# Performance work log

Hardware: AMD Instinct MI355X
Metric: run time of the kernel (lower is better)

The kernel has to match this reference:

```python
import jax, jax.numpy as jnp
from jax import lax
import numpy as np

B, T, H = 4096, 512, 32


def _rnn_layer(xs, h0, Wih, Whh, bih, bhh):
    # xs: [T, B, in], h0: [B, H]. torch RNN tanh: h_t = tanh(x W_ih^T + b_ih + h W_hh^T + b_hh)
    def step(h, x_t):
        h = jnp.tanh(x_t @ Wih.T + bih + h @ Whh.T + bhh)
        return h, h
    h_last, ys = lax.scan(step, h0, xs)
    return ys, h_last  # ys: [T, B, H]


def setup_inputs() -> dict:
    key = jax.random.key(0)
    ks = jax.random.split(key, 12)
    s = 0.1  # keep tanh out of saturation
    return {
        "x": jax.random.normal(ks[0], (B, T, 1), jnp.float32),
        "h_state": jnp.zeros((2, B, H), jnp.float32),
        "Wih0": jax.random.normal(ks[1], (H, 1), jnp.float32) * s,
        "Whh0": jax.random.normal(ks[2], (H, H), jnp.float32) * s,
        "bih0": jax.random.normal(ks[3], (H,), jnp.float32) * s,
        "bhh0": jax.random.normal(ks[4], (H,), jnp.float32) * s,
        "Wih1": jax.random.normal(ks[5], (H, H), jnp.float32) * s,
        "Whh1": jax.random.normal(ks[6], (H, H), jnp.float32) * s,
        "bih1": jax.random.normal(ks[7], (H,), jnp.float32) * s,
        "bhh1": jax.random.normal(ks[8], (H,), jnp.float32) * s,
        "Wfc": jax.random.normal(ks[9], (1, H), jnp.float32) * s,
        "bfc": jax.random.normal(ks[10], (1,), jnp.float32) * s,
    }


def reference(x, h_state, Wih0, Whh0, bih0, bhh0, Wih1, Whh1, bih1, bhh1, Wfc, bfc):
    xs = jnp.transpose(x, (1, 0, 2))  # time-major [T, B, 1]
    ys0, h0_last = _rnn_layer(xs, h_state[0], Wih0, Whh0, bih0, bhh0)
    ys1, h1_last = _rnn_layer(ys0, h_state[1], Wih1, Whh1, bih1, bhh1)
    last = ys1[-1]                      # [B, H] == r_out[:, -1, :]
    pred = (last @ Wfc.T + bfc)[:, 0]   # Linear(32,1) then squeeze(-1) -> [B]
    h_new = jnp.stack([h0_last, h1_last], axis=0)  # [2, B, H]
    return pred, h_new
```

## Files before the change

### kernel.cpp

```cpp
#include <hip/hip_runtime.h>

#define BB 4096
#define TT 512
#define HH 32

typedef _Float16 half8 __attribute__((ext_vector_type(8)));
typedef _Float16 half4 __attribute__((ext_vector_type(4)));
typedef _Float16 h2    __attribute__((ext_vector_type(2)));
typedef float    f32x4 __attribute__((ext_vector_type(4)));

#define MFMA16F(a, b, c) __builtin_amdgcn_mfma_f32_16x16x32_f16((a), (b), (c), 0, 0, 0)

union frag_u { half8 h8; h2 p[4]; };
union h4u   { half4 v;  h2 p[2]; };

__device__ __forceinline__ h2 pkrtz(float a, float b) {
    auto r = __builtin_amdgcn_cvt_pkrtz(a, b);
    union { decltype(r) i; h2 o; } u;
    u.i = r;
    return u.o;
}

__device__ __forceinline__ h2 tanh_h2(h2 v) {
    const h2 LO = {(_Float16)(-2.75f), (_Float16)(-2.75f)};
    const h2 HI = {(_Float16)(2.75f), (_Float16)(2.75f)};
    const h2 C0 = {(_Float16)(0.9976293f), (_Float16)(0.9976293f)};
    const h2 C1 = {(_Float16)(-0.3098016f), (_Float16)(-0.3098016f)};
    const h2 C2 = {(_Float16)(0.0889744f), (_Float16)(0.0889744f)};
    const h2 C3 = {(_Float16)(-0.0163448f), (_Float16)(-0.0163448f)};
    const h2 C4 = {(_Float16)(0.0016113f), (_Float16)(0.0016113f)};
    const h2 C5 = {(_Float16)(-0.00006405f), (_Float16)(-0.00006405f)};
    v = __builtin_elementwise_min(v, HI);
    v = __builtin_elementwise_max(v, LO);
    h2 u = v * v;
    h2 t = __builtin_elementwise_fma(u, C5, C4);
    t = __builtin_elementwise_fma(u, t, C3);
    t = __builtin_elementwise_fma(u, t, C2);
    t = __builtin_elementwise_fma(u, t, C1);
    t = __builtin_elementwise_fma(u, t, C0);
    return v * t;
}

#define XBAR()                                                    \
    do {                                                          \
        asm volatile("s_waitcnt lgkmcnt(0)" ::: "memory");        \
        __builtin_amdgcn_s_barrier();                             \
        asm volatile("" ::: "memory");                            \
    } while (0)

__global__ __launch_bounds__(128) void rnn2_mfma_hs(
    const float* __restrict__ x,
    const float* __restrict__ hstate,
    const float* __restrict__ Wih0,
    const float* __restrict__ Whh0,
    const float* __restrict__ bih0,
    const float* __restrict__ bhh0,
    const float* __restrict__ Wih1,
    const float* __restrict__ Whh1,
    const float* __restrict__ bih1,
    const float* __restrict__ bhh1,
    const float* __restrict__ Wfc,
    const float* __restrict__ bfc,
    float* __restrict__ out)
{
    const int tid = threadIdx.x;
    const int l = tid & 63;
    const int wid = __builtin_amdgcn_readfirstlane(tid >> 6);
    const int q = l >> 4;
    const int n = l & 15;
    const int b = blockIdx.x * 16 + n;
    const bool w0 = (wid == 0);

    __shared__ half4 xbH[2][2][64];

    const int r0 = 8 * (n >> 2) + (n & 3);
    half8 A1i[2], A1h[2];
#pragma unroll
    for (int t = 0; t < 2; ++t) {
        const int row = r0 + 4 * t;
        const float* p1 = Wih1 + row * HH + q * 8;
        const float* p2 = Whh1 + row * HH + q * 8;
        frag_u f1, f2;
#pragma unroll
        for (int jj = 0; jj < 4; ++jj) {
            f1.p[jj] = h2{(_Float16)p1[2 * jj], (_Float16)p1[2 * jj + 1]};
            f2.p[jj] = h2{(_Float16)p2[2 * jj], (_Float16)p2[2 * jj + 1]};
        }
        A1i[t] = f1.h8; A1h[t] = f2.h8;
    }
    half8 A0w;
    {
        const int row = r0 + 4 * wid;
        const float* p0 = Whh0 + row * HH + q * 8;
        frag_u f0;
#pragma unroll
        for (int jj = 0; jj < 4; ++jj)
            f0.p[jj] = h2{(_Float16)p0[2 * jj], (_Float16)p0[2 * jj + 1]};
        A0w = f0.h8;
    }

    float wxs[4], b0s[4], wfc8[8];
#pragma unroll
    for (int r = 0; r < 4; ++r) {
        const int hh = 8 * q + 4 * wid + r;
        wxs[r] = Wih0[hh];
        b0s[r] = bih0[hh] + bhh0[hh];
    }
    f32x4 c1t0, c1t1;
#pragma unroll
    for (int r = 0; r < 4; ++r) {
        c1t0[r] = bih1[8 * q + r] + bhh1[8 * q + r];
        c1t1[r] = bih1[8 * q + 4 + r] + bhh1[8 * q + 4 + r];
    }
#pragma unroll
    for (int j = 0; j < 8; ++j) wfc8[j] = Wfc[8 * q + j];

    frag_u hb0, hb1;
    {
        const float* p0 = hstate + (size_t)b * HH + 8 * q;
        const float* p1 = hstate + (size_t)BB * HH + (size_t)b * HH + 8 * q;
#pragma unroll
        for (int jj = 0; jj < 4; ++jj) {
            hb0.p[jj] = h2{(_Float16)p0[2 * jj], (_Float16)p0[2 * jj + 1]};
            hb1.p[jj] = h2{(_Float16)p1[2 * jj], (_Float16)p1[2 * jj + 1]};
        }
    }

    f32x4 dbp0 = MFMA16F(A1h[0], hb1.h8, c1t0);
    f32x4 dbp1 = MFMA16F(A1h[1], hb1.h8, c1t1);

    const float4* xp = (const float4*)(x + (size_t)b * TT);
    float4 xc = xp[0];

    {
        f32x4 c0;
#pragma unroll
        for (int r = 0; r < 4; ++r) c0[r] = fmaf(wxs[r], xc.x, b0s[r]);
        f32x4 d0 = MFMA16F(A0w, hb0.h8, c0);
        h4u ho;
        ho.p[0] = tanh_h2(pkrtz(d0[0], d0[1]));
        ho.p[1] = tanh_h2(pkrtz(d0[2], d0[3]));
        xbH[wid][0][l] = ho.v;
        XBAR();
        h4u lo, hi;
        lo.v = xbH[0][0][l];
        hi.v = xbH[1][0][l];
        hb0.p[0] = lo.p[0]; hb0.p[1] = lo.p[1];
        hb0.p[2] = hi.p[0]; hb0.p[3] = hi.p[1];
    }

#define STEPB(XT, SLOT)                                                       \
    {                                                                         \
        f32x4 d10 = MFMA16F(A1i[0], hb0.h8, dbp0);                            \
        f32x4 d11 = MFMA16F(A1i[1], hb0.h8, dbp1);                            \
        f32x4 c0;                                                             \
        _Pragma("unroll")                                                     \
        for (int r = 0; r < 4; ++r) c0[r] = fmaf(wxs[r], (XT), b0s[r]);       \
        f32x4 d0 = MFMA16F(A0w, hb0.h8, c0);                                  \
        h4u ho;                                                               \
        ho.p[0] = tanh_h2(pkrtz(d0[0], d0[1]));                               \
        ho.p[1] = tanh_h2(pkrtz(d0[2], d0[3]));                               \
        xbH[wid][SLOT][l] = ho.v;                                             \
        XBAR();                                                               \
        h4u lo, hi;                                                           \
        lo.v = xbH[0][SLOT][l];                                               \
        hi.v = xbH[1][SLOT][l];                                               \
        hb1.p[0] = tanh_h2(pkrtz(d10[0], d10[1]));                            \
        hb1.p[1] = tanh_h2(pkrtz(d10[2], d10[3]));                            \
        hb1.p[2] = tanh_h2(pkrtz(d11[0], d11[1]));                            \
        hb1.p[3] = tanh_h2(pkrtz(d11[2], d11[3]));                            \
        dbp0 = MFMA16F(A1h[0], hb1.h8, c1t0);                                 \
        dbp1 = MFMA16F(A1h[1], hb1.h8, c1t1);                                 \
        hb0.p[0] = lo.p[0]; hb0.p[1] = lo.p[1];                               \
        hb0.p[2] = hi.p[0]; hb0.p[3] = hi.p[1];                               \
    }

    for (int k = 0; k < TT / 4 - 1; ++k) {
        float4 xn = xp[k + 1];
        STEPB(xc.y, 1);
        STEPB(xc.z, 0);
        STEPB(xc.w, 1);
        STEPB(xn.x, 0);
        xc = xn;
    }
    STEPB(xc.y, 1);
    STEPB(xc.z, 0);
    STEPB(xc.w, 1);

    {
        f32x4 d10 = MFMA16F(A1i[0], hb0.h8, dbp0);
        f32x4 d11 = MFMA16F(A1i[1], hb0.h8, dbp1);
        hb1.p[0] = tanh_h2(pkrtz(d10[0], d10[1]));
        hb1.p[1] = tanh_h2(pkrtz(d10[2], d10[3]));
        hb1.p[2] = tanh_h2(pkrtz(d11[0], d11[1]));
        hb1.p[3] = tanh_h2(pkrtz(d11[2], d11[3]));
    }

    float hf0[8], hf1[8];
#pragma unroll
    for (int jj = 0; jj < 4; ++jj) {
        hf0[2 * jj]     = (float)hb0.p[jj].x;
        hf0[2 * jj + 1] = (float)hb0.p[jj].y;
        hf1[2 * jj]     = (float)hb1.p[jj].x;
        hf1[2 * jj + 1] = (float)hb1.p[jj].y;
    }
    if (w0) {
#pragma unroll
        for (int j = 0; j < 8; ++j)
            out[BB + (size_t)b * HH + 8 * q + j] = hf0[j];
    } else {
        float p = 0.f;
#pragma unroll
        for (int j = 0; j < 8; ++j) p = fmaf(wfc8[j], hf1[j], p);
        p += __shfl_xor(p, 16);
        p += __shfl_xor(p, 32);
        if (q == 0) out[b] = p + bfc[0];
#pragma unroll
        for (int j = 0; j < 8; ++j)
            out[BB + (size_t)BB * HH + (size_t)b * HH + 8 * q + j] = hf1[j];
    }
}

extern "C" void kernel_launch(void* const* d_in, const int* in_sizes, int n_in,
                              void* d_out, int out_size, void* d_ws, size_t ws_size,
                              hipStream_t stream) {
    const float* x      = (const float*)d_in[0];
    const float* hstate = (const float*)d_in[1];
    const float* Wih0   = (const float*)d_in[2];
    const float* Whh0   = (const float*)d_in[3];
    const float* bih0   = (const float*)d_in[4];
    const float* bhh0   = (const float*)d_in[5];
    const float* Wih1   = (const float*)d_in[6];
    const float* Whh1   = (const float*)d_in[7];
    const float* bih1   = (const float*)d_in[8];
    const float* bhh1   = (const float*)d_in[9];
    const float* Wfc    = (const float*)d_in[10];
    const float* bfc    = (const float*)d_in[11];
    float* out = (float*)d_out;

    dim3 grid(BB / 16);
    dim3 block(128);
    hipLaunchKernelGGL(rnn2_mfma_hs, grid, block, 0, stream,
                       x, hstate, Wih0, Whh0, bih0, bhh0,
                       Wih1, Whh1, bih1, bhh1, Wfc, bfc, out);
}
```

Before: 204.6 us.

## Split layer-1 recurrence onto a dedicated third wave per block

Blocks grow from two waves to three. Waves 0 and 1 each compute half of the layer-0 hidden state. Wave 2 alone runs the layer-1 MFMAs and tanh on the layer-0 state from the previous step, so the two layers run as a wavefront pipeline. The aim is to take layer-1 work off the critical path of the layer-0 waves at each barrier. In exchange, each block has 50% more waves, wave 2 writes an unused LDS slot every step, and all three waves must still meet at the per-step barrier.

```diff
diff --git a/kernel.cpp b/kernel.cpp
--- a/kernel.cpp
+++ b/kernel.cpp
@@ -48,7 +48,7 @@
         asm volatile("" ::: "memory");                            \
     } while (0)
 
-__global__ __launch_bounds__(128) void rnn2_mfma_hs(
+__global__ __launch_bounds__(192) void rnn2_mfma_pc(
     const float* __restrict__ x,
     const float* __restrict__ hstate,
     const float* __restrict__ Wih0,
@@ -69,11 +69,22 @@
     const int q = l >> 4;
     const int n = l & 15;
     const int b = blockIdx.x * 16 + n;
-    const bool w0 = (wid == 0);
-
-    __shared__ half4 xbH[2][2][64];
+    const bool w2 = (wid == 2);
+
+    __shared__ half4 xbH[3][2][64];
 
     const int r0 = 8 * (n >> 2) + (n & 3);
+    const int ot = wid & 1;
+    half8 A0w;
+    {
+        const int row = r0 + 4 * ot;
+        const float* p0 = Whh0 + row * HH + q * 8;
+        frag_u f0;
+#pragma unroll
+        for (int jj = 0; jj < 4; ++jj)
+            f0.p[jj] = h2{(_Float16)p0[2 * jj], (_Float16)p0[2 * jj + 1]};
+        A0w = f0.h8;
+    }
     half8 A1i[2], A1h[2];
 #pragma unroll
     for (int t = 0; t < 2; ++t) {
@@ -88,21 +99,11 @@
         }
         A1i[t] = f1.h8; A1h[t] = f2.h8;
     }
-    half8 A0w;
-    {
-        const int row = r0 + 4 * wid;
-        const float* p0 = Whh0 + row * HH + q * 8;
-        frag_u f0;
-#pragma unroll
-        for (int jj = 0; jj < 4; ++jj)
-            f0.p[jj] = h2{(_Float16)p0[2 * jj], (_Float16)p0[2 * jj + 1]};
-        A0w = f0.h8;
-    }
 
     float wxs[4], b0s[4], wfc8[8];
 #pragma unroll
     for (int r = 0; r < 4; ++r) {
-        const int hh = 8 * q + 4 * wid + r;
+        const int hh = 8 * q + 4 * ot + r;
         wxs[r] = Wih0[hh];
         b0s[r] = bih0[hh] + bhh0[hh];
     }
@@ -115,17 +116,16 @@
 #pragma unroll
     for (int j = 0; j < 8; ++j) wfc8[j] = Wfc[8 * q + j];
 
-    frag_u hb0, hb1;
+    frag_u hb0full, hb1;
     {
         const float* p0 = hstate + (size_t)b * HH + 8 * q;
         const float* p1 = hstate + (size_t)BB * HH + (size_t)b * HH + 8 * q;
 #pragma unroll
         for (int jj = 0; jj < 4; ++jj) {
-            hb0.p[jj] = h2{(_Float16)p0[2 * jj], (_Float16)p0[2 * jj + 1]};
-            hb1.p[jj] = h2{(_Float16)p1[2 * jj], (_Float16)p1[2 * jj + 1]};
-        }
-    }
-
+            hb0full.p[jj] = h2{(_Float16)p0[2 * jj], (_Float16)p0[2 * jj + 1]};
+            hb1.p[jj]     = h2{(_Float16)p1[2 * jj], (_Float16)p1[2 * jj + 1]};
+        }
+    }
     f32x4 dbp0 = MFMA16F(A1h[0], hb1.h8, c1t0);
     f32x4 dbp1 = MFMA16F(A1h[1], hb1.h8, c1t1);
 
@@ -133,46 +133,51 @@
     float4 xc = xp[0];
 
     {
-        f32x4 c0;
-#pragma unroll
-        for (int r = 0; r < 4; ++r) c0[r] = fmaf(wxs[r], xc.x, b0s[r]);
-        f32x4 d0 = MFMA16F(A0w, hb0.h8, c0);
-        h4u ho;
-        ho.p[0] = tanh_h2(pkrtz(d0[0], d0[1]));
-        ho.p[1] = tanh_h2(pkrtz(d0[2], d0[3]));
-        xbH[wid][0][l] = ho.v;
+        h4u wout = {};
+        if (!w2) {
+            f32x4 c0;
+#pragma unroll
+            for (int r = 0; r < 4; ++r) c0[r] = fmaf(wxs[r], xc.x, b0s[r]);
+            f32x4 d0 = MFMA16F(A0w, hb0full.h8, c0);
+            wout.p[0] = tanh_h2(pkrtz(d0[0], d0[1]));
+            wout.p[1] = tanh_h2(pkrtz(d0[2], d0[3]));
+        }
+        xbH[wid][0][l] = wout.v;
         XBAR();
         h4u lo, hi;
         lo.v = xbH[0][0][l];
         hi.v = xbH[1][0][l];
-        hb0.p[0] = lo.p[0]; hb0.p[1] = lo.p[1];
-        hb0.p[2] = hi.p[0]; hb0.p[3] = hi.p[1];
+        hb0full.p[0] = lo.p[0]; hb0full.p[1] = lo.p[1];
+        hb0full.p[2] = hi.p[0]; hb0full.p[3] = hi.p[1];
     }
 
 #define STEPB(XT, SLOT)                                                       \
     {                                                                         \
-        f32x4 d10 = MFMA16F(A1i[0], hb0.h8, dbp0);                            \
-        f32x4 d11 = MFMA16F(A1i[1], hb0.h8, dbp1);                            \
-        f32x4 c0;                                                             \
-        _Pragma("unroll")                                                     \
-        for (int r = 0; r < 4; ++r) c0[r] = fmaf(wxs[r], (XT), b0s[r]);       \
-        f32x4 d0 = MFMA16F(A0w, hb0.h8, c0);                                  \
-        h4u ho;                                                               \
-        ho.p[0] = tanh_h2(pkrtz(d0[0], d0[1]));                               \
-        ho.p[1] = tanh_h2(pkrtz(d0[2], d0[3]));                               \
-        xbH[wid][SLOT][l] = ho.v;                                             \
+        h4u wout = {};                                                        \
+        if (w2) {                                                             \
+            f32x4 d10 = MFMA16F(A1i[0], hb0full.h8, dbp0);                    \
+            f32x4 d11 = MFMA16F(A1i[1], hb0full.h8, dbp1);                    \
+            hb1.p[0] = tanh_h2(pkrtz(d10[0], d10[1]));                        \
+            hb1.p[1] = tanh_h2(pkrtz(d10[2], d10[3]));                        \
+            hb1.p[2] = tanh_h2(pkrtz(d11[0], d11[1]));                        \
+            hb1.p[3] = tanh_h2(pkrtz(d11[2], d11[3]));                        \
+            dbp0 = MFMA16F(A1h[0], hb1.h8, c1t0);                             \
+            dbp1 = MFMA16F(A1h[1], hb1.h8, c1t1);                             \
+        } else {                                                              \
+            f32x4 c0;                                                         \
+            _Pragma("unroll")                                                 \
+            for (int r = 0; r < 4; ++r) c0[r] = fmaf(wxs[r], (XT), b0s[r]);   \
+            f32x4 d0 = MFMA16F(A0w, hb0full.h8, c0);                          \
+            wout.p[0] = tanh_h2(pkrtz(d0[0], d0[1]));                         \
+            wout.p[1] = tanh_h2(pkrtz(d0[2], d0[3]));                         \
+        }                                                                     \
+        xbH[wid][SLOT][l] = wout.v;                                           \
         XBAR();                                                               \
         h4u lo, hi;                                                           \
         lo.v = xbH[0][SLOT][l];                                               \
         hi.v = xbH[1][SLOT][l];                                               \
-        hb1.p[0] = tanh_h2(pkrtz(d10[0], d10[1]));                            \
-        hb1.p[1] = tanh_h2(pkrtz(d10[2], d10[3]));                            \
-        hb1.p[2] = tanh_h2(pkrtz(d11[0], d11[1]));                            \
-        hb1.p[3] = tanh_h2(pkrtz(d11[2], d11[3]));                            \
-        dbp0 = MFMA16F(A1h[0], hb1.h8, c1t0);                                 \
-        dbp1 = MFMA16F(A1h[1], hb1.h8, c1t1);                                 \
-        hb0.p[0] = lo.p[0]; hb0.p[1] = lo.p[1];                               \
-        hb0.p[2] = hi.p[0]; hb0.p[3] = hi.p[1];                               \
+        hb0full.p[0] = lo.p[0]; hb0full.p[1] = lo.p[1];                       \
+        hb0full.p[2] = hi.p[0]; hb0full.p[3] = hi.p[1];                       \
     }
 
     for (int k = 0; k < TT / 4 - 1; ++k) {
@@ -187,28 +192,28 @@
     STEPB(xc.z, 0);
     STEPB(xc.w, 1);
 
-    {
-        f32x4 d10 = MFMA16F(A1i[0], hb0.h8, dbp0);
-        f32x4 d11 = MFMA16F(A1i[1], hb0.h8, dbp1);
+    if (w2) {
+        f32x4 d10 = MFMA16F(A1i[0], hb0full.h8, dbp0);
+        f32x4 d11 = MFMA16F(A1i[1], hb0full.h8, dbp1);
         hb1.p[0] = tanh_h2(pkrtz(d10[0], d10[1]));
         hb1.p[1] = tanh_h2(pkrtz(d10[2], d10[3]));
         hb1.p[2] = tanh_h2(pkrtz(d11[0], d11[1]));
         hb1.p[3] = tanh_h2(pkrtz(d11[2], d11[3]));
     }
 
-    float hf0[8], hf1[8];
-#pragma unroll
-    for (int jj = 0; jj < 4; ++jj) {
-        hf0[2 * jj]     = (float)hb0.p[jj].x;
-        hf0[2 * jj + 1] = (float)hb0.p[jj].y;
-        hf1[2 * jj]     = (float)hb1.p[jj].x;
-        hf1[2 * jj + 1] = (float)hb1.p[jj].y;
-    }
-    if (w0) {
-#pragma unroll
-        for (int j = 0; j < 8; ++j)
-            out[BB + (size_t)b * HH + 8 * q + j] = hf0[j];
-    } else {
+    if (wid == 0) {
+#pragma unroll
+        for (int jj = 0; jj < 4; ++jj) {
+            out[BB + (size_t)b * HH + 8 * q + 2 * jj]     = (float)hb0full.p[jj].x;
+            out[BB + (size_t)b * HH + 8 * q + 2 * jj + 1] = (float)hb0full.p[jj].y;
+        }
+    } else if (w2) {
+        float hf1[8];
+#pragma unroll
+        for (int jj = 0; jj < 4; ++jj) {
+            hf1[2 * jj]     = (float)hb1.p[jj].x;
+            hf1[2 * jj + 1] = (float)hb1.p[jj].y;
+        }
         float p = 0.f;
 #pragma unroll
         for (int j = 0; j < 8; ++j) p = fmaf(wfc8[j], hf1[j], p);
@@ -239,8 +244,8 @@
     float* out = (float*)d_out;
 
     dim3 grid(BB / 16);
-    dim3 block(128);
-    hipLaunchKernelGGL(rnn2_mfma_hs, grid, block, 0, stream,
+    dim3 block(192);
+    hipLaunchKernelGGL(rnn2_mfma_pc, grid, block, 0, stream,
                        x, hstate, Wih0, Whh0, bih0, bhh0,
                        Wih1, Whh1, bih1, bhh1, Wfc, bfc, out);
 }
```

Measured after the change: 216.8 us. +5.9%, slower.

## Split layer-1 input projection and recurrence across the two waves via LDS

Applied to the files above, without the earlier changes.

Wave 0 now computes the layer-1 input projection (Wih1·h0 + bias) and passes it through shared memory. Wave 1 consumes it one step later and does only the Whh1 recurrence and tanh. Before, both waves redundantly computed all four layer-1 MFMAs every step. The aim is to shorten each wave's per-step critical path and balance the work across waves. The cost is extra LDS writes and reads of f32x4 partials each step, plus a one-step pipeline skew that adds prologue and epilogue barriers.

```diff
diff --git a/kernel.cpp b/kernel.cpp
--- a/kernel.cpp
+++ b/kernel.cpp
@@ -48,7 +48,7 @@
         asm volatile("" ::: "memory");                            \
     } while (0)
 
-__global__ __launch_bounds__(128) void rnn2_mfma_hs(
+__global__ __launch_bounds__(128) void rnn2_mfma_es(
     const float* __restrict__ x,
     const float* __restrict__ hstate,
     const float* __restrict__ Wih0,
@@ -72,6 +72,7 @@
     const bool w0 = (wid == 0);
 
     __shared__ half4 xbH[2][2][64];
+    __shared__ f32x4 xbE[2][2][2][64];
 
     const int r0 = 8 * (n >> 2) + (n & 3);
     half8 A1i[2], A1h[2];
@@ -126,8 +127,8 @@
         }
     }
 
-    f32x4 dbp0 = MFMA16F(A1h[0], hb1.h8, c1t0);
-    f32x4 dbp1 = MFMA16F(A1h[1], hb1.h8, c1t1);
+    const f32x4 zz = {0.f, 0.f, 0.f, 0.f};
+    f32x4 eC0 = zz, eC1 = zz;
 
     const float4* xp = (const float4*)(x + (size_t)b * TT);
     float4 xc = xp[0];
@@ -141,6 +142,8 @@
         ho.p[0] = tanh_h2(pkrtz(d0[0], d0[1]));
         ho.p[1] = tanh_h2(pkrtz(d0[2], d0[3]));
         xbH[wid][0][l] = ho.v;
+        xbE[wid][0][0][l] = zz;
+        xbE[wid][0][1][l] = zz;
         XBAR();
         h4u lo, hi;
         lo.v = xbH[0][0][l];
@@ -148,11 +151,46 @@
         hb0.p[0] = lo.p[0]; hb0.p[1] = lo.p[1];
         hb0.p[2] = hi.p[0]; hb0.p[3] = hi.p[1];
     }
-
-#define STEPB(XT, SLOT)                                                       \
+    {
+        f32x4 en0v = zz, en1v = zz;
+        if (w0) {
+            en0v = MFMA16F(A1i[0], hb0.h8, c1t0);
+            en1v = MFMA16F(A1i[1], hb0.h8, c1t1);
+        }
+        f32x4 c0;
+#pragma unroll
+        for (int r = 0; r < 4; ++r) c0[r] = fmaf(wxs[r], xc.y, b0s[r]);
+        f32x4 d0 = MFMA16F(A0w, hb0.h8, c0);
+        h4u ho;
+        ho.p[0] = tanh_h2(pkrtz(d0[0], d0[1]));
+        ho.p[1] = tanh_h2(pkrtz(d0[2], d0[3]));
+        xbH[wid][1][l] = ho.v;
+        xbE[wid][1][0][l] = en0v;
+        xbE[wid][1][1][l] = en1v;
+        XBAR();
+        h4u lo, hi;
+        lo.v = xbH[0][1][l];
+        hi.v = xbH[1][1][l];
+        hb0.p[0] = lo.p[0]; hb0.p[1] = lo.p[1];
+        hb0.p[2] = hi.p[0]; hb0.p[3] = hi.p[1];
+        eC0 = xbE[0][1][0][l];
+        eC1 = xbE[0][1][1][l];
+    }
+
+#define STEPE(XT, SLOT)                                                       \
     {                                                                         \
-        f32x4 d10 = MFMA16F(A1i[0], hb0.h8, dbp0);                            \
-        f32x4 d11 = MFMA16F(A1i[1], hb0.h8, dbp1);                            \
+        f32x4 en0v = zz, en1v = zz;                                           \
+        if (w0) {                                                             \
+            en0v = MFMA16F(A1i[0], hb0.h8, c1t0);                             \
+            en1v = MFMA16F(A1i[1], hb0.h8, c1t1);                             \
+        } else {                                                              \
+            f32x4 d10 = MFMA16F(A1h[0], hb1.h8, eC0);                         \
+            f32x4 d11 = MFMA16F(A1h[1], hb1.h8, eC1);                         \
+            hb1.p[0] = tanh_h2(pkrtz(d10[0], d10[1]));                        \
+            hb1.p[1] = tanh_h2(pkrtz(d10[2], d10[3]));                        \
+            hb1.p[2] = tanh_h2(pkrtz(d11[0], d11[1]));                        \
+            hb1.p[3] = tanh_h2(pkrtz(d11[2], d11[3]));                        \
+        }                                                                     \
         f32x4 c0;                                                             \
         _Pragma("unroll")                                                     \
         for (int r = 0; r < 4; ++r) c0[r] = fmaf(wxs[r], (XT), b0s[r]);       \
@@ -161,54 +199,70 @@
         ho.p[0] = tanh_h2(pkrtz(d0[0], d0[1]));                               \
         ho.p[1] = tanh_h2(pkrtz(d0[2], d0[3]));                               \
         xbH[wid][SLOT][l] = ho.v;                                             \
+        xbE[wid][SLOT][0][l] = en0v;                                          \
+        xbE[wid][SLOT][1][l] = en1v;                                          \
         XBAR();                                                               \
         h4u lo, hi;                                                           \
         lo.v = xbH[0][SLOT][l];                                               \
         hi.v = xbH[1][SLOT][l];                                               \
-        hb1.p[0] = tanh_h2(pkrtz(d10[0], d10[1]));                            \
-        hb1.p[1] = tanh_h2(pkrtz(d10[2], d10[3]));                            \
-        hb1.p[2] = tanh_h2(pkrtz(d11[0], d11[1]));                            \
-        hb1.p[3] = tanh_h2(pkrtz(d11[2], d11[3]));                            \
-        dbp0 = MFMA16F(A1h[0], hb1.h8, c1t0);                                 \
-        dbp1 = MFMA16F(A1h[1], hb1.h8, c1t1);                                 \
         hb0.p[0] = lo.p[0]; hb0.p[1] = lo.p[1];                               \
         hb0.p[2] = hi.p[0]; hb0.p[3] = hi.p[1];                               \
+        eC0 = xbE[0][SLOT][0][l];                                             \
+        eC1 = xbE[0][SLOT][1][l];                                             \
     }
 
     for (int k = 0; k < TT / 4 - 1; ++k) {
         float4 xn = xp[k + 1];
-        STEPB(xc.y, 1);
-        STEPB(xc.z, 0);
-        STEPB(xc.w, 1);
-        STEPB(xn.x, 0);
+        STEPE(xc.z, 0);
+        STEPE(xc.w, 1);
+        STEPE(xn.x, 0);
+        STEPE(xn.y, 1);
         xc = xn;
     }
-    STEPB(xc.y, 1);
-    STEPB(xc.z, 0);
-    STEPB(xc.w, 1);
-
-    {
-        f32x4 d10 = MFMA16F(A1i[0], hb0.h8, dbp0);
-        f32x4 d11 = MFMA16F(A1i[1], hb0.h8, dbp1);
+    STEPE(xc.z, 0);
+    STEPE(xc.w, 1);
+
+    {
+        f32x4 en0v = zz, en1v = zz;
+        if (w0) {
+            en0v = MFMA16F(A1i[0], hb0.h8, c1t0);
+            en1v = MFMA16F(A1i[1], hb0.h8, c1t1);
+        } else {
+            f32x4 d10 = MFMA16F(A1h[0], hb1.h8, eC0);
+            f32x4 d11 = MFMA16F(A1h[1], hb1.h8, eC1);
+            hb1.p[0] = tanh_h2(pkrtz(d10[0], d10[1]));
+            hb1.p[1] = tanh_h2(pkrtz(d10[2], d10[3]));
+            hb1.p[2] = tanh_h2(pkrtz(d11[0], d11[1]));
+            hb1.p[3] = tanh_h2(pkrtz(d11[2], d11[3]));
+        }
+        xbE[wid][0][0][l] = en0v;
+        xbE[wid][0][1][l] = en1v;
+        XBAR();
+        eC0 = xbE[0][0][0][l];
+        eC1 = xbE[0][0][1][l];
+    }
+    if (!w0) {
+        f32x4 d10 = MFMA16F(A1h[0], hb1.h8, eC0);
+        f32x4 d11 = MFMA16F(A1h[1], hb1.h8, eC1);
         hb1.p[0] = tanh_h2(pkrtz(d10[0], d10[1]));
         hb1.p[1] = tanh_h2(pkrtz(d10[2], d10[3]));
         hb1.p[2] = tanh_h2(pkrtz(d11[0], d11[1]));
         hb1.p[3] = tanh_h2(pkrtz(d11[2], d11[3]));
     }
 
-    float hf0[8], hf1[8];
-#pragma unroll
-    for (int jj = 0; jj < 4; ++jj) {
-        hf0[2 * jj]     = (float)hb0.p[jj].x;
-        hf0[2 * jj + 1] = (float)hb0.p[jj].y;
-        hf1[2 * jj]     = (float)hb1.p[jj].x;
-        hf1[2 * jj + 1] = (float)hb1.p[jj].y;
-    }
     if (w0) {
 #pragma unroll
-        for (int j = 0; j < 8; ++j)
-            out[BB + (size_t)b * HH + 8 * q + j] = hf0[j];
+        for (int jj = 0; jj < 4; ++jj) {
+            out[BB + (size_t)b * HH + 8 * q + 2 * jj]     = (float)hb0.p[jj].x;
+            out[BB + (size_t)b * HH + 8 * q + 2 * jj + 1] = (float)hb0.p[jj].y;
+        }
     } else {
+        float hf1[8];
+#pragma unroll
+        for (int jj = 0; jj < 4; ++jj) {
+            hf1[2 * jj]     = (float)hb1.p[jj].x;
+            hf1[2 * jj + 1] = (float)hb1.p[jj].y;
+        }
         float p = 0.f;
 #pragma unroll
         for (int j = 0; j < 8; ++j) p = fmaf(wfc8[j], hf1[j], p);
@@ -240,7 +294,7 @@
 
     dim3 grid(BB / 16);
     dim3 block(128);
-    hipLaunchKernelGGL(rnn2_mfma_hs, grid, block, 0, stream,
+    hipLaunchKernelGGL(rnn2_mfma_es, grid, block, 0, stream,
                        x, hstate, Wih0, Whh0, bih0, bhh0,
                        Wih1, Whh1, bih1, bhh1, Wfc, bfc, out);
 }
```

Result: slower. 271.9 us (+32.9%).

## Split layer-1 RNN rows across both waves and exchange halves via LDS

Applied to the files above, without the earlier changes.

Layer 1 was computed redundantly by both waves, each doing two Whh1 and two Wih1 MFMAs per step. Now each wave owns half of the layer-1 hidden rows, does one MFMA of each, and swaps its half with the other wave through a second LDS buffer at the same barrier used for layer 0. This halves per-step layer-1 MFMA and tanh work per wave. In exchange it adds LDS writes and reads per step, and the Whh1 and Wih1 MFMAs now sit back to back on the critical path, where before the Whh1 product was precomputed one step ahead.

```diff
diff --git a/kernel.cpp b/kernel.cpp
--- a/kernel.cpp
+++ b/kernel.cpp
@@ -48,7 +48,7 @@
         asm volatile("" ::: "memory");                            \
     } while (0)
 
-__global__ __launch_bounds__(128) void rnn2_mfma_hs(
+__global__ __launch_bounds__(128) void rnn2_mfma_ds(
     const float* __restrict__ x,
     const float* __restrict__ hstate,
     const float* __restrict__ Wih0,
@@ -71,46 +71,34 @@
     const int b = blockIdx.x * 16 + n;
     const bool w0 = (wid == 0);
 
-    __shared__ half4 xbH[2][2][64];
+    __shared__ half4 xh0[2][2][64];
+    __shared__ half4 xh1[2][2][64];
 
     const int r0 = 8 * (n >> 2) + (n & 3);
-    half8 A1i[2], A1h[2];
-#pragma unroll
-    for (int t = 0; t < 2; ++t) {
-        const int row = r0 + 4 * t;
+    const int row = r0 + 4 * wid;
+    half8 A0w, A1iw, A1hw;
+    {
+        const float* p0 = Whh0 + row * HH + q * 8;
         const float* p1 = Wih1 + row * HH + q * 8;
         const float* p2 = Whh1 + row * HH + q * 8;
-        frag_u f1, f2;
-#pragma unroll
-        for (int jj = 0; jj < 4; ++jj) {
+        frag_u f0, f1, f2;
+#pragma unroll
+        for (int jj = 0; jj < 4; ++jj) {
+            f0.p[jj] = h2{(_Float16)p0[2 * jj], (_Float16)p0[2 * jj + 1]};
             f1.p[jj] = h2{(_Float16)p1[2 * jj], (_Float16)p1[2 * jj + 1]};
             f2.p[jj] = h2{(_Float16)p2[2 * jj], (_Float16)p2[2 * jj + 1]};
         }
-        A1i[t] = f1.h8; A1h[t] = f2.h8;
-    }
-    half8 A0w;
-    {
-        const int row = r0 + 4 * wid;
-        const float* p0 = Whh0 + row * HH + q * 8;
-        frag_u f0;
-#pragma unroll
-        for (int jj = 0; jj < 4; ++jj)
-            f0.p[jj] = h2{(_Float16)p0[2 * jj], (_Float16)p0[2 * jj + 1]};
-        A0w = f0.h8;
+        A0w = f0.h8; A1iw = f1.h8; A1hw = f2.h8;
     }
 
     float wxs[4], b0s[4], wfc8[8];
+    f32x4 c1H;
 #pragma unroll
     for (int r = 0; r < 4; ++r) {
         const int hh = 8 * q + 4 * wid + r;
         wxs[r] = Wih0[hh];
         b0s[r] = bih0[hh] + bhh0[hh];
-    }
-    f32x4 c1t0, c1t1;
-#pragma unroll
-    for (int r = 0; r < 4; ++r) {
-        c1t0[r] = bih1[8 * q + r] + bhh1[8 * q + r];
-        c1t1[r] = bih1[8 * q + 4 + r] + bhh1[8 * q + 4 + r];
+        c1H[r] = bih1[hh] + bhh1[hh];
     }
 #pragma unroll
     for (int j = 0; j < 8; ++j) wfc8[j] = Wfc[8 * q + j];
@@ -126,9 +114,6 @@
         }
     }
 
-    f32x4 dbp0 = MFMA16F(A1h[0], hb1.h8, c1t0);
-    f32x4 dbp1 = MFMA16F(A1h[1], hb1.h8, c1t1);
-
     const float4* xp = (const float4*)(x + (size_t)b * TT);
     float4 xc = xp[0];
 
@@ -137,78 +122,90 @@
 #pragma unroll
         for (int r = 0; r < 4; ++r) c0[r] = fmaf(wxs[r], xc.x, b0s[r]);
         f32x4 d0 = MFMA16F(A0w, hb0.h8, c0);
-        h4u ho;
-        ho.p[0] = tanh_h2(pkrtz(d0[0], d0[1]));
-        ho.p[1] = tanh_h2(pkrtz(d0[2], d0[3]));
-        xbH[wid][0][l] = ho.v;
+        h4u o0;
+        o0.p[0] = tanh_h2(pkrtz(d0[0], d0[1]));
+        o0.p[1] = tanh_h2(pkrtz(d0[2], d0[3]));
+        xh0[wid][0][l] = o0.v;
         XBAR();
-        h4u lo, hi;
-        lo.v = xbH[0][0][l];
-        hi.v = xbH[1][0][l];
-        hb0.p[0] = lo.p[0]; hb0.p[1] = lo.p[1];
-        hb0.p[2] = hi.p[0]; hb0.p[3] = hi.p[1];
-    }
-
-#define STEPB(XT, SLOT)                                                       \
+        h4u t0;
+        t0.v = xh0[wid ^ 1][0][l];
+        hb0.p[0] = w0 ? o0.p[0] : t0.p[0];
+        hb0.p[1] = w0 ? o0.p[1] : t0.p[1];
+        hb0.p[2] = w0 ? t0.p[0] : o0.p[0];
+        hb0.p[3] = w0 ? t0.p[1] : o0.p[1];
+    }
+
+#define STEPD(XT, SLOT)                                                       \
     {                                                                         \
-        f32x4 d10 = MFMA16F(A1i[0], hb0.h8, dbp0);                            \
-        f32x4 d11 = MFMA16F(A1i[1], hb0.h8, dbp1);                            \
+        f32x4 dbpH = MFMA16F(A1hw, hb1.h8, c1H);                              \
+        f32x4 d1 = MFMA16F(A1iw, hb0.h8, dbpH);                               \
         f32x4 c0;                                                             \
         _Pragma("unroll")                                                     \
         for (int r = 0; r < 4; ++r) c0[r] = fmaf(wxs[r], (XT), b0s[r]);       \
         f32x4 d0 = MFMA16F(A0w, hb0.h8, c0);                                  \
-        h4u ho;                                                               \
-        ho.p[0] = tanh_h2(pkrtz(d0[0], d0[1]));                               \
-        ho.p[1] = tanh_h2(pkrtz(d0[2], d0[3]));                               \
-        xbH[wid][SLOT][l] = ho.v;                                             \
+        h4u o1;                                                               \
+        o1.p[0] = tanh_h2(pkrtz(d1[0], d1[1]));                               \
+        o1.p[1] = tanh_h2(pkrtz(d1[2], d1[3]));                               \
+        xh1[wid][SLOT][l] = o1.v;                                             \
+        h4u o0;                                                               \
+        o0.p[0] = tanh_h2(pkrtz(d0[0], d0[1]));                               \
+        o0.p[1] = tanh_h2(pkrtz(d0[2], d0[3]));                               \
+        xh0[wid][SLOT][l] = o0.v;                                             \
         XBAR();                                                               \
-        h4u lo, hi;                                                           \
-        lo.v = xbH[0][SLOT][l];                                               \
-        hi.v = xbH[1][SLOT][l];                                               \
-        hb1.p[0] = tanh_h2(pkrtz(d10[0], d10[1]));                            \
-        hb1.p[1] = tanh_h2(pkrtz(d10[2], d10[3]));                            \
-        hb1.p[2] = tanh_h2(pkrtz(d11[0], d11[1]));                            \
-        hb1.p[3] = tanh_h2(pkrtz(d11[2], d11[3]));                            \
-        dbp0 = MFMA16F(A1h[0], hb1.h8, c1t0);                                 \
-        dbp1 = MFMA16F(A1h[1], hb1.h8, c1t1);                                 \
-        hb0.p[0] = lo.p[0]; hb0.p[1] = lo.p[1];                               \
-        hb0.p[2] = hi.p[0]; hb0.p[3] = hi.p[1];                               \
+        h4u t1, t0;                                                           \
+        t1.v = xh1[wid ^ 1][SLOT][l];                                         \
+        t0.v = xh0[wid ^ 1][SLOT][l];                                         \
+        hb1.p[0] = w0 ? o1.p[0] : t1.p[0];                                    \
+        hb1.p[1] = w0 ? o1.p[1] : t1.p[1];                                    \
+        hb1.p[2] = w0 ? t1.p[0] : o1.p[0];                                    \
+        hb1.p[3] = w0 ? t1.p[1] : o1.p[1];                                    \
+        hb0.p[0] = w0 ? o0.p[0] : t0.p[0];                                    \
+        hb0.p[1] = w0 ? o0.p[1] : t0.p[1];                                    \
+        hb0.p[2] = w0 ? t0.p[0] : o0.p[0];                                    \
+        hb0.p[3] = w0 ? t0.p[1] : o0.p[1];                                    \
     }
 
     for (int k = 0; k < TT / 4 - 1; ++k) {
         float4 xn = xp[k + 1];
-        STEPB(xc.y, 1);
-        STEPB(xc.z, 0);
-        STEPB(xc.w, 1);
-        STEPB(xn.x, 0);
+        STEPD(xc.y, 1);
+        STEPD(xc.z, 0);
+        STEPD(xc.w, 1);
+        STEPD(xn.x, 0);
         xc = xn;
     }
-    STEPB(xc.y, 1);
-    STEPB(xc.z, 0);
-    STEPB(xc.w, 1);
-
-    {
-        f32x4 d10 = MFMA16F(A1i[0], hb0.h8, dbp0);
-        f32x4 d11 = MFMA16F(A1i[1], hb0.h8, dbp1);
-        hb1.p[0] = tanh_h2(pkrtz(d10[0], d10[1]));
-        hb1.p[1] = tanh_h2(pkrtz(d10[2], d10[3]));
-        hb1.p[2] = tanh_h2(pkrtz(d11[0], d11[1]));
-        hb1.p[3] = tanh_h2(pkrtz(d11[2], d11[3]));
-    }
-
-    float hf0[8], hf1[8];
-#pragma unroll
-    for (int jj = 0; jj < 4; ++jj) {
-        hf0[2 * jj]     = (float)hb0.p[jj].x;
-        hf0[2 * jj + 1] = (float)hb0.p[jj].y;
-        hf1[2 * jj]     = (float)hb1.p[jj].x;
-        hf1[2 * jj + 1] = (float)hb1.p[jj].y;
-    }
+    STEPD(xc.y, 1);
+    STEPD(xc.z, 0);
+    STEPD(xc.w, 1);
+
+    {
+        f32x4 dbpH = MFMA16F(A1hw, hb1.h8, c1H);
+        f32x4 d1 = MFMA16F(A1iw, hb0.h8, dbpH);
+        h4u o1;
+        o1.p[0] = tanh_h2(pkrtz(d1[0], d1[1]));
+        o1.p[1] = tanh_h2(pkrtz(d1[2], d1[3]));
+        xh1[wid][0][l] = o1.v;
+        XBAR();
+        h4u t1;
+        t1.v = xh1[wid ^ 1][0][l];
+        hb1.p[0] = w0 ? o1.p[0] : t1.p[0];
+        hb1.p[1] = w0 ? o1.p[1] : t1.p[1];
+        hb1.p[2] = w0 ? t1.p[0] : o1.p[0];
+        hb1.p[3] = w0 ? t1.p[1] : o1.p[1];
+    }
+
     if (w0) {
 #pragma unroll
-        for (int j = 0; j < 8; ++j)
-            out[BB + (size_t)b * HH + 8 * q + j] = hf0[j];
+        for (int jj = 0; jj < 4; ++jj) {
+            out[BB + (size_t)b * HH + 8 * q + 2 * jj]     = (float)hb0.p[jj].x;
+            out[BB + (size_t)b * HH + 8 * q + 2 * jj + 1] = (float)hb0.p[jj].y;
+        }
     } else {
+        float hf1[8];
+#pragma unroll
+        for (int jj = 0; jj < 4; ++jj) {
+            hf1[2 * jj]     = (float)hb1.p[jj].x;
+            hf1[2 * jj + 1] = (float)hb1.p[jj].y;
+        }
         float p = 0.f;
 #pragma unroll
         for (int j = 0; j < 8; ++j) p = fmaf(wfc8[j], hf1[j], p);
@@ -240,7 +237,7 @@
 
     dim3 grid(BB / 16);
     dim3 block(128);
-    hipLaunchKernelGGL(rnn2_mfma_hs, grid, block, 0, stream,
+    hipLaunchKernelGGL(rnn2_mfma_ds, grid, block, 0, stream,
                        x, hstate, Wih0, Whh0, bih0, bhh0,
                        Wih1, Whh1, bih1, bhh1, Wfc, bfc, out);
 }
```

After: 218.6 us. 1.07x slower.
